# Kernel optimization log

Hardware: AMD Instinct MI355X
Metric: run time of the kernel (lower is better)

## Reference

```python
import jax, jax.numpy as jnp
import numpy as np

B, S, D, U = 4, 2048, 1024, 1024

def setup_inputs() -> dict:
    key = jax.random.key(0)
    k0, k1, k2, k3 = jax.random.split(key, 4)
    scale = 1.0 / np.sqrt(D)  # keep logits sane; Glorot-like magnitude
    return {
        "inputs": jax.random.normal(k0, (B, S, D), dtype=jnp.float32),
        "W_q": jax.random.normal(k1, (D, U), dtype=jnp.float32) * scale,
        "W_k": jax.random.normal(k2, (D, U), dtype=jnp.float32) * scale,
        "W_v": jax.random.normal(k3, (D, U), dtype=jnp.float32) * scale,
    }

def reference(inputs, W_q, W_k, W_v):
    # QKV projections: [B,S,D] @ [D,U] -> [B,S,U]
    q = jnp.einsum("bsd,du->bsu", inputs, W_q)
    k = jnp.einsum("bsd,du->bsu", inputs, W_k)
    v = jnp.einsum("bsd,du->bsu", inputs, W_v)
    # Unscaled attention, as in the source (no 1/sqrt(d) factor)
    scores = jnp.einsum("bqu,bku->bqk", q, k)          # [B,S,S]
    weights = jax.nn.softmax(scores, axis=-1)
    return jnp.einsum("bqk,bku->bqu", weights, v)       # [B,S,U]
```

## Files before the change

kernel.cpp:

```cpp
#include <hip/hip_runtime.h>
#include <cstdint>
#include <cstddef>


typedef unsigned short ushort_t;
typedef _Float16 half_t;
typedef __attribute__((ext_vector_type(8))) short short8;
typedef __attribute__((ext_vector_type(4))) float floatx4;

__device__ inline unsigned short h2u(half_t h) {
  union { half_t h; unsigned short u; } v; v.h = h; return v.u;
}

__device__ __forceinline__ void gload16(const half_t* g, half_t* l) {
  __builtin_amdgcn_global_load_lds(
      (const __attribute__((address_space(1))) unsigned int*)g,
      (__attribute__((address_space(3))) unsigned int*)l, 16, 0, 0);
}

#define BAR() asm volatile("s_barrier" ::: "memory")
#define LGKM0() asm volatile("s_waitcnt lgkmcnt(0)" ::: "memory")
#define VM6() asm volatile("s_waitcnt vmcnt(6)" ::: "memory")
#define VM0() asm volatile("s_waitcnt vmcnt(0)" ::: "memory")

#define MX 8192
#define KCAT 2048

#define XCAT_OFF 0UL
#define WT_OFF   50331648UL
#define S_OFF    0UL
#define QCAT_OFF 69206016UL
#define KCAT_OFF 119537664UL
#define VT_OFF   169869312UL
#define WS_NEED  186646528UL

__global__ __launch_bounds__(256) void k_split_x(const float* __restrict__ X,
                                                 half_t* __restrict__ xcat) {
  long long i = (long long)blockIdx.x * 256 + threadIdx.x;
  float x = X[i];
  half_t h = (half_t)x;
  half_t lo = (half_t)(x - (float)h);
  long long row = i >> 10;
  int col = (int)(i & 1023);
  half_t* r = xcat + row * KCAT;
  r[col] = h;
  r[col + 1024] = lo;
}

__global__ __launch_bounds__(256) void k_split_wt(const float* __restrict__ Wq,
                                                  const float* __restrict__ Wk,
                                                  const float* __restrict__ Wv,
                                                  half_t* __restrict__ wt) {
  __shared__ float tile[64][65];
  const float* W = (blockIdx.z == 0) ? Wq : ((blockIdx.z == 1) ? Wk : Wv);
  half_t* out = wt + (size_t)blockIdx.z * 1024 * KCAT;
  int d0 = blockIdx.y * 64, u0 = blockIdx.x * 64;
  int t = threadIdx.x;
  int tr = t >> 6, tc = t & 63;
  for (int r = 0; r < 64; r += 4)
    tile[r + tr][tc] = W[(size_t)(d0 + r + tr) * 1024 + (u0 + tc)];
  __syncthreads();
  for (int r = 0; r < 64; r += 4) {
    int urow = r + tr, dcol = tc;
    float x = tile[dcol][urow];
    half_t h = (half_t)x;
    half_t* o = out + (size_t)(u0 + urow) * KCAT + d0;
    o[dcol] = h;
    o[dcol + 1024] = h;
  }
}

enum { EP_F32 = 0, EP_QK = 1, EP_VT = 2 };

template <int MODE>
__global__ __launch_bounds__(256, 4) void k_gemm(
    const half_t* __restrict__ A, long long aBatch, int lda,
    const half_t* __restrict__ Bt, long long bBatch, int ldb,
    void* __restrict__ Cout, long long cBatch, int ldc, int K,
    half_t* __restrict__ CoutK) {
  __shared__ __align__(16) half_t As[128 * 64];
  __shared__ __align__(16) half_t Bs[128 * 64];
  const int t = threadIdx.x;
  const int z = blockIdx.z;
  A += (long long)z * aBatch;
  Bt += (long long)z * bBatch;
  const int m0 = blockIdx.y * 128, n0 = blockIdx.x * 128;

  const int w = t >> 6, l = t & 63;
  const int lr = l & 15, quad = l >> 4;
  const int wm = (w >> 1) * 64, wn = (w & 1) * 64;

  const floatx4 fz = {0.f, 0.f, 0.f, 0.f};
  floatx4 acc[4][4];
#pragma unroll
  for (int i = 0; i < 4; i++)
#pragma unroll
    for (int j = 0; j < 4; j++) acc[i][j] = fz;

  const half_t* Ap[4];
  const half_t* Bp[4];
  half_t* ldsA[4];
  half_t* ldsB[4];
#pragma unroll
  for (int s = 0; s < 4; s++) {
    int c = s * 256 + t;
    int row = c >> 3, gq = (c & 7) ^ ((c >> 3) & 7);
    Ap[s] = A + (long long)(m0 + row) * lda + gq * 8;
    Bp[s] = Bt + (long long)(n0 + row) * ldb + gq * 8;
    ldsA[s] = &As[(s * 256 + w * 64) * 8];
    ldsB[s] = &Bs[(s * 256 + w * 64) * 8];
  }

  const int p0 = quad ^ (lr & 7);
  const int p1 = (quad + 4) ^ (lr & 7);
  const int arow = (wm + lr) * 64, brow = (wn + lr) * 64;

  for (int kb = 0; kb < K; kb += 64) {
    __syncthreads();
#pragma unroll
    for (int s = 0; s < 4; s++) {
      gload16(Ap[s] + kb, ldsA[s]);
      gload16(Bp[s] + kb, ldsB[s]);
    }
    __syncthreads();
#pragma unroll
    for (int s = 0; s < 2; s++) {
      const int pp = s ? p1 : p0;
      short8 af[4], bfg[4];
#pragma unroll
      for (int j = 0; j < 4; j++) bfg[j] = *(const short8*)&Bs[brow + j * 1024 + pp * 8];
#pragma unroll
      for (int i = 0; i < 4; i++) af[i] = *(const short8*)&As[arow + i * 1024 + pp * 8];
#pragma unroll
      for (int i = 0; i < 4; i++)
#pragma unroll
        for (int j = 0; j < 4; j++)
          acc[i][j] = __builtin_amdgcn_mfma_f32_16x16x32_f16(af[i], bfg[j], acc[i][j], 0, 0, 0);
    }
  }

#pragma unroll
  for (int i = 0; i < 4; i++) {
#pragma unroll
    for (int j = 0; j < 4; j++) {
#pragma unroll
      for (int r = 0; r < 4; r++) {
        int grow = m0 + wm + i * 16 + quad * 4 + r;
        int gcol = n0 + wn + j * 16 + lr;
        float v = acc[i][j][r];
        if (MODE == EP_F32) {
          float* C = (float*)Cout + (long long)z * cBatch;
          C[(long long)grow * ldc + gcol] = v;
        } else if (MODE == EP_QK) {
          int sel = gcol >> 10;
          int ucol = gcol & 1023;
          half_t h = (half_t)v;
          if (sel == 0) {
            half_t* pq = (half_t*)Cout + (long long)grow * KCAT;
            pq[ucol] = h;
            pq[ucol + 1024] = (half_t)(v - (float)h);
          } else {
            half_t* pk = CoutK + (long long)grow * KCAT;
            pk[ucol] = h;
            pk[ucol + 1024] = h;
          }
        } else {
          half_t* C = (half_t*)Cout;
          int b = grow >> 11, s = grow & 2047;
          C[((long long)b * 1024 + gcol) * 2048 + s] = (half_t)v;
        }
      }
    }
  }
}

template <int MODE>
__global__ __launch_bounds__(512, 2) void k_gemm256(
    const half_t* __restrict__ A, long long aBatch, int lda,
    const half_t* __restrict__ Bt, long long bBatch, int ldb,
    void* __restrict__ Cout, long long cBatch, int ldc, int K,
    half_t* __restrict__ CoutK) {
  __shared__ __align__(16) half_t As[32768];
  __shared__ __align__(16) half_t Bs[32768];
  const int tid = threadIdx.x;
  const int z = blockIdx.z;
  A += (long long)z * aBatch;
  Bt += (long long)z * bBatch;
  const int m0 = blockIdx.y * 256, n0 = blockIdx.x * 256;
  const int w = tid >> 6, l = tid & 63;
  const int lr = l & 15, quad = l >> 4;
  const int wm = w >> 2, wn = w & 3;

  const floatx4 fz = {0.f, 0.f, 0.f, 0.f};
  floatx4 acc[8][4];
#pragma unroll
  for (int i = 0; i < 8; i++)
#pragma unroll
    for (int j = 0; j < 4; j++) acc[i][j] = fz;

  const int r0 = tid >> 2;
  const int gq0 = (tid & 3) ^ ((tid >> 3) & 3);
  const half_t* aS0 = A + (long long)(m0 + r0) * lda + gq0 * 8;
  const half_t* aS1 = aS0 + (long long)128 * lda;
  const half_t* bS0 = Bt + (long long)(n0 + r0) * ldb + gq0 * 8;
  const half_t* bS1 = bS0 + (long long)128 * ldb;
  const int wso = w << 9;

  const int swz = (quad ^ ((lr >> 1) & 3)) << 3;
  const int aBase = wm * 4096 + lr * 32 + swz;
  const int bBase = wn * 2048 + lr * 32 + swz;
  const int NT = K >> 6;

#define SA(BUF, KH, KOFF) do { half_t* d_ = &As[(BUF) * 16384 + (KH) * 8192 + wso]; \
    gload16(aS0 + (KOFF), d_); gload16(aS1 + (KOFF), d_ + 4096); } while (0)
#define SB(BUF, KH, KOFF) do { half_t* d_ = &Bs[(BUF) * 16384 + (KH) * 8192 + wso]; \
    gload16(bS0 + (KOFF), d_); gload16(bS1 + (KOFF), d_ + 4096); } while (0)
#define LDA4(OFF) { const half_t* ap_ = &As[(OFF)]; \
    af0 = *(const short8*)(ap_); af1 = *(const short8*)(ap_ + 512); \
    af2 = *(const short8*)(ap_ + 1024); af3 = *(const short8*)(ap_ + 1536); }
#define LDB4(OFF) { const half_t* bp_ = &Bs[(OFF)]; \
    bf0 = *(const short8*)(bp_); bf1 = *(const short8*)(bp_ + 512); \
    bf2 = *(const short8*)(bp_ + 1024); bf3 = *(const short8*)(bp_ + 1536); }
#define MFMA16(I0) do { \
    acc[(I0) + 0][0] = __builtin_amdgcn_mfma_f32_16x16x32_f16(af0, bf0, acc[(I0) + 0][0], 0, 0, 0); \
    acc[(I0) + 0][1] = __builtin_amdgcn_mfma_f32_16x16x32_f16(af0, bf1, acc[(I0) + 0][1], 0, 0, 0); \
    acc[(I0) + 0][2] = __builtin_amdgcn_mfma_f32_16x16x32_f16(af0, bf2, acc[(I0) + 0][2], 0, 0, 0); \
    acc[(I0) + 0][3] = __builtin_amdgcn_mfma_f32_16x16x32_f16(af0, bf3, acc[(I0) + 0][3], 0, 0, 0); \
    acc[(I0) + 1][0] = __builtin_amdgcn_mfma_f32_16x16x32_f16(af1, bf0, acc[(I0) + 1][0], 0, 0, 0); \
    acc[(I0) + 1][1] = __builtin_amdgcn_mfma_f32_16x16x32_f16(af1, bf1, acc[(I0) + 1][1], 0, 0, 0); \
    acc[(I0) + 1][2] = __builtin_amdgcn_mfma_f32_16x16x32_f16(af1, bf2, acc[(I0) + 1][2], 0, 0, 0); \
    acc[(I0) + 1][3] = __builtin_amdgcn_mfma_f32_16x16x32_f16(af1, bf3, acc[(I0) + 1][3], 0, 0, 0); \
    acc[(I0) + 2][0] = __builtin_amdgcn_mfma_f32_16x16x32_f16(af2, bf0, acc[(I0) + 2][0], 0, 0, 0); \
    acc[(I0) + 2][1] = __builtin_amdgcn_mfma_f32_16x16x32_f16(af2, bf1, acc[(I0) + 2][1], 0, 0, 0); \
    acc[(I0) + 2][2] = __builtin_amdgcn_mfma_f32_16x16x32_f16(af2, bf2, acc[(I0) + 2][2], 0, 0, 0); \
    acc[(I0) + 2][3] = __builtin_amdgcn_mfma_f32_16x16x32_f16(af2, bf3, acc[(I0) + 2][3], 0, 0, 0); \
    acc[(I0) + 3][0] = __builtin_amdgcn_mfma_f32_16x16x32_f16(af3, bf0, acc[(I0) + 3][0], 0, 0, 0); \
    acc[(I0) + 3][1] = __builtin_amdgcn_mfma_f32_16x16x32_f16(af3, bf1, acc[(I0) + 3][1], 0, 0, 0); \
    acc[(I0) + 3][2] = __builtin_amdgcn_mfma_f32_16x16x32_f16(af3, bf2, acc[(I0) + 3][2], 0, 0, 0); \
    acc[(I0) + 3][3] = __builtin_amdgcn_mfma_f32_16x16x32_f16(af3, bf3, acc[(I0) + 3][3], 0, 0, 0); \
  } while (0)

  SB(0, 0, 0); SA(0, 0, 0); SB(0, 1, 32); SA(0, 1, 32);
  SB(1, 0, 64); SA(1, 0, 64); SB(1, 1, 96);
  VM6();
  BAR();

  for (int t = 0; t < NT; ++t) {
    const int buf = t & 1, nbuf = buf ^ 1;
    const int ab = buf * 16384;
    const int kb = t * 64;
    short8 af0, af1, af2, af3, bf0, bf1, bf2, bf3;

    LDA4(ab + aBase);
    LDB4(ab + bBase);
    if (t + 1 < NT) SA(nbuf, 1, kb + 96);
    BAR(); LGKM0();
    __builtin_amdgcn_s_setprio(1); MFMA16(0); __builtin_amdgcn_s_setprio(0);
    BAR();

    LDA4(ab + aBase + 2048);
    if (t + 2 < NT) SB(buf, 0, kb + 128);
    BAR(); LGKM0();
    __builtin_amdgcn_s_setprio(1); MFMA16(4); __builtin_amdgcn_s_setprio(0);
    BAR();

    LDA4(ab + 8192 + aBase);
    LDB4(ab + 8192 + bBase);
    if (t + 2 < NT) SA(buf, 0, kb + 128);
    BAR(); LGKM0();
    __builtin_amdgcn_s_setprio(1); MFMA16(0); __builtin_amdgcn_s_setprio(0);
    BAR();

    LDA4(ab + 8192 + aBase + 2048);
    if (t + 2 < NT) SB(buf, 1, kb + 160);
    if (t < NT - 2) { VM6(); } else if (t == NT - 2) { VM0(); }
    BAR(); LGKM0();
    __builtin_amdgcn_s_setprio(1); MFMA16(4); __builtin_amdgcn_s_setprio(0);
    BAR();
  }

#pragma unroll
  for (int i = 0; i < 8; i++) {
#pragma unroll
    for (int j = 0; j < 4; j++) {
#pragma unroll
      for (int r = 0; r < 4; r++) {
        int grow = m0 + wm * 128 + i * 16 + quad * 4 + r;
        int gcol = n0 + wn * 64 + j * 16 + lr;
        float v = acc[i][j][r];
        if (MODE == EP_F32) {
          float* C = (float*)Cout + (long long)z * cBatch;
          C[(long long)grow * ldc + gcol] = v;
        } else {
          int sel = gcol >> 10;
          int ucol = gcol & 1023;
          half_t h = (half_t)v;
          if (sel == 0) {
            half_t* pq = (half_t*)Cout + (long long)grow * KCAT;
            pq[ucol] = h;
            pq[ucol + 1024] = (half_t)(v - (float)h);
          } else {
            half_t* pk = CoutK + (long long)grow * KCAT;
            pk[ucol] = h;
            pk[ucol + 1024] = h;
          }
        }
      }
    }
  }
#undef SA
#undef SB
#undef LDA4
#undef LDB4
#undef MFMA16
}

__global__ __launch_bounds__(256) void k_softmax(float* __restrict__ Sbuf) {
  long long row = blockIdx.x;
  float* p = Sbuf + row * 2048;
  int t = threadIdx.x;
  float4 v0 = ((const float4*)p)[t];
  float4 v1 = ((const float4*)p)[t + 256];
  float m = fmaxf(fmaxf(fmaxf(v0.x, v0.y), fmaxf(v0.z, v0.w)),
                  fmaxf(fmaxf(v1.x, v1.y), fmaxf(v1.z, v1.w)));
  for (int off = 32; off; off >>= 1) m = fmaxf(m, __shfl_xor(m, off));
  __shared__ float red[8];
  int wv = t >> 6, ln = t & 63;
  if (ln == 0) red[wv] = m;
  __syncthreads();
  m = fmaxf(fmaxf(red[0], red[1]), fmaxf(red[2], red[3]));
  float e0 = __expf(v0.x - m), e1 = __expf(v0.y - m), e2 = __expf(v0.z - m), e3 = __expf(v0.w - m);
  float e4 = __expf(v1.x - m), e5 = __expf(v1.y - m), e6 = __expf(v1.z - m), e7 = __expf(v1.w - m);
  float s = ((e0 + e1) + (e2 + e3)) + ((e4 + e5) + (e6 + e7));
  for (int off = 32; off; off >>= 1) s += __shfl_xor(s, off);
  if (ln == 0) red[4 + wv] = s;
  __syncthreads();
  s = (red[4] + red[5]) + (red[6] + red[7]);
  float inv = 1.0f / s;
  uint2 w0, w1;
  w0.x = (unsigned)h2u((half_t)(e0 * inv)) | ((unsigned)h2u((half_t)(e1 * inv)) << 16);
  w0.y = (unsigned)h2u((half_t)(e2 * inv)) | ((unsigned)h2u((half_t)(e3 * inv)) << 16);
  w1.x = (unsigned)h2u((half_t)(e4 * inv)) | ((unsigned)h2u((half_t)(e5 * inv)) << 16);
  w1.y = (unsigned)h2u((half_t)(e6 * inv)) | ((unsigned)h2u((half_t)(e7 * inv)) << 16);
  ((uint2*)p)[t] = w0;
  ((uint2*)p)[t + 256] = w1;
}

extern "C" void kernel_launch(void* const* d_in, const int* in_sizes, int n_in,
                              void* d_out, int out_size, void* d_ws, size_t ws_size,
                              hipStream_t stream) {
  (void)in_sizes; (void)n_in; (void)out_size;
  if (ws_size < WS_NEED) return;

  const float* X = (const float*)d_in[0];
  const float* Wq = (const float*)d_in[1];
  const float* Wk = (const float*)d_in[2];
  const float* Wv = (const float*)d_in[3];
  char* ws = (char*)d_ws;
  half_t* xcat = (half_t*)(ws + XCAT_OFF);
  half_t* wt = (half_t*)(ws + WT_OFF);
  float* Sbuf = (float*)(ws + S_OFF);
  half_t* qcat = (half_t*)(ws + QCAT_OFF);
  half_t* kcat = (half_t*)(ws + KCAT_OFF);
  half_t* vt = (half_t*)(ws + VT_OFF);
  float* out = (float*)d_out;

  k_split_x<<<dim3(MX * 1024 / 256), dim3(256), 0, stream>>>(X, xcat);
  k_split_wt<<<dim3(16, 16, 3), dim3(256), 0, stream>>>(Wq, Wk, Wv, wt);

  k_gemm256<EP_QK><<<dim3(8, 32, 1), dim3(512), 0, stream>>>(
      xcat, 0LL, KCAT, wt, 0LL, KCAT, qcat, 0LL, 0, KCAT, kcat);

  k_gemm<EP_VT><<<dim3(8, 64, 1), dim3(256), 0, stream>>>(
      xcat, 0LL, KCAT, wt + 2 * 1024 * KCAT, 0LL, KCAT, vt, 0LL, 0, 1024, nullptr);

  k_gemm256<EP_F32><<<dim3(8, 8, 4), dim3(512), 0, stream>>>(
      qcat, (long long)2048 * KCAT, KCAT, kcat, (long long)2048 * KCAT, KCAT,
      Sbuf, (long long)2048 * 2048, 2048, KCAT, nullptr);

  k_softmax<<<dim3(8192), dim3(256), 0, stream>>>(Sbuf);

  k_gemm<EP_F32><<<dim3(8, 16, 4), dim3(256), 0, stream>>>(
      (const half_t*)Sbuf, (long long)2048 * 4096, 4096,
      vt, (long long)1024 * 2048, 2048,
      out, (long long)2048 * 1024, 1024, 2048, nullptr);
}
```

Measured before the change: 336.7 us.

## Stage GEMM epilogues through LDS and split-K the PV GEMM with atomics

The 256x256 GEMM epilogue now stages accumulators through swizzled LDS so the Q/K and fp32 score outputs are written with wide vectorized stores instead of scattered scalar stores. The final weights-times-V GEMM moves from the 128-tile kernel to the 256-tile kernel, with K split in two across blockIdx.z and partial sums combined into a pre-zeroed output via atomicAdd. This targets poor store coalescing and low tile reuse in the final GEMM. The cost is an extra zeroing pass, atomic traffic on the output, and an accumulation order that is no longer deterministic.

```diff
diff --git a/kernel.cpp b/kernel.cpp
--- a/kernel.cpp
+++ b/kernel.cpp
@@ -33,6 +33,13 @@
 #define KCAT_OFF 119537664UL
 #define VT_OFF   169869312UL
 #define WS_NEED  186646528UL
+
+__global__ __launch_bounds__(256) void k_zero(float* __restrict__ p, long long n4) {
+  long long i = (long long)blockIdx.x * 256 + threadIdx.x;
+  const floatx4 z = {0.f, 0.f, 0.f, 0.f};
+  long long stride = (long long)gridDim.x * 256;
+  for (; i < n4; i += stride) ((floatx4*)p)[i] = z;
+}
 
 __global__ __launch_bounds__(256) void k_split_x(const float* __restrict__ X,
                                                  half_t* __restrict__ xcat) {
@@ -70,7 +77,7 @@
   }
 }
 
-enum { EP_F32 = 0, EP_QK = 1, EP_VT = 2 };
+enum { EP_F32 = 0, EP_QK = 1, EP_VT = 2, EP_ATOMIC = 3 };
 
 template <int MODE>
 __global__ __launch_bounds__(256, 4) void k_gemm(
@@ -180,12 +187,15 @@
     const half_t* __restrict__ Bt, long long bBatch, int ldb,
     void* __restrict__ Cout, long long cBatch, int ldc, int K,
     half_t* __restrict__ CoutK) {
-  __shared__ __align__(16) half_t As[32768];
-  __shared__ __align__(16) half_t Bs[32768];
+  __shared__ __align__(16) half_t LDS[65536];
+  half_t* As = LDS;
+  half_t* Bs = LDS + 32768;
   const int tid = threadIdx.x;
   const int z = blockIdx.z;
-  A += (long long)z * aBatch;
-  Bt += (long long)z * bBatch;
+  int zb = z, kOff = 0;
+  if (MODE == EP_ATOMIC) { zb = z >> 1; kOff = (z & 1) * 1024; }
+  A += (long long)zb * aBatch + kOff;
+  Bt += (long long)zb * bBatch + kOff;
   const int m0 = blockIdx.y * 256, n0 = blockIdx.x * 256;
   const int w = tid >> 6, l = tid & 63;
   const int lr = l & 15, quad = l >> 4;
@@ -279,34 +289,79 @@
     BAR();
   }
 
-#pragma unroll
-  for (int i = 0; i < 8; i++) {
-#pragma unroll
-    for (int j = 0; j < 4; j++) {
-#pragma unroll
-      for (int r = 0; r < 4; r++) {
-        int grow = m0 + wm * 128 + i * 16 + quad * 4 + r;
-        int gcol = n0 + wn * 64 + j * 16 + lr;
-        float v = acc[i][j][r];
-        if (MODE == EP_F32) {
-          float* C = (float*)Cout + (long long)z * cBatch;
-          C[(long long)grow * ldc + gcol] = v;
-        } else {
-          int sel = gcol >> 10;
-          int ucol = gcol & 1023;
-          half_t h = (half_t)v;
-          if (sel == 0) {
-            half_t* pq = (half_t*)Cout + (long long)grow * KCAT;
-            pq[ucol] = h;
-            pq[ucol + 1024] = (half_t)(v - (float)h);
-          } else {
-            half_t* pk = CoutK + (long long)grow * KCAT;
-            pk[ucol] = h;
-            pk[ucol + 1024] = h;
+  BAR();
+  half_t* wreg = &LDS[w * 8192];
+
+  if (MODE == EP_QK) {
+    const int sel = n0 >> 10;
+    const int ncol0 = (n0 & 1023) + wn * 64;
+    half_t* dbase = (sel == 0) ? (half_t*)Cout : CoutK;
+    const long long rb = (long long)(m0 + wm * 128);
+#pragma unroll
+    for (int round = 0; round < 2; ++round) {
+#pragma unroll
+      for (int i = 0; i < 8; i++)
+#pragma unroll
+        for (int j = 0; j < 4; j++)
+#pragma unroll
+          for (int r = 0; r < 4; r++) {
+            int row = i * 16 + quad * 4 + r;
+            int col = j * 16 + lr;
+            float v = acc[i][j][r];
+            half_t hv = (half_t)v;
+            half_t val = (round == 0) ? hv
+                         : (sel == 0 ? (half_t)(v - (float)hv) : hv);
+            wreg[row * 64 + (((col >> 3) ^ (row & 7)) << 3) + (col & 7)] = val;
           }
-        }
+#pragma unroll
+      for (int k2 = 0; k2 < 16; ++k2) {
+        int cid = l + 64 * k2;
+        int row = cid >> 3, q = cid & 7;
+        short8 vv = *(const short8*)&wreg[row * 64 + ((q ^ (row & 7)) << 3)];
+        half_t* dst = dbase + (rb + row) * KCAT + ncol0 + q * 8 + round * 1024;
+        *(short8*)dst = vv;
       }
     }
+  } else if (MODE == EP_F32) {
+    float* wreg32 = (float*)wreg;
+    float* C = (float*)Cout + (long long)zb * cBatch;
+#pragma unroll
+    for (int hh = 0; hh < 2; ++hh) {
+#pragma unroll
+      for (int i2 = 0; i2 < 4; i2++)
+#pragma unroll
+        for (int j = 0; j < 4; j++)
+#pragma unroll
+          for (int r = 0; r < 4; r++) {
+            int i = hh * 4 + i2;
+            int row64 = i2 * 16 + quad * 4 + r;
+            int col = j * 16 + lr;
+            int c4 = col >> 2;
+            wreg32[row64 * 64 + ((c4 ^ (row64 & 7)) << 2) + (col & 3)] =
+                acc[i][j][r];
+          }
+      long long rbase = (long long)(m0 + wm * 128 + hh * 64);
+#pragma unroll
+      for (int k2 = 0; k2 < 16; ++k2) {
+        int cid = l + 64 * k2;
+        int row64 = cid >> 4, q = cid & 15;
+        floatx4 vv = *(const floatx4*)&wreg32[row64 * 64 + ((q ^ (row64 & 7)) << 2)];
+        float* dst = C + (rbase + row64) * ldc + n0 + wn * 64 + q * 4;
+        *(floatx4*)dst = vv;
+      }
+    }
+  } else {
+    float* C = (float*)Cout + (long long)zb * cBatch;
+#pragma unroll
+    for (int i = 0; i < 8; i++)
+#pragma unroll
+      for (int j = 0; j < 4; j++)
+#pragma unroll
+        for (int r = 0; r < 4; r++) {
+          int grow = m0 + wm * 128 + i * 16 + quad * 4 + r;
+          int gcol = n0 + wn * 64 + j * 16 + lr;
+          atomicAdd(&C[(long long)grow * ldc + gcol], acc[i][j][r]);
+        }
   }
 #undef SA
 #undef SB
@@ -365,6 +420,8 @@
   half_t* vt = (half_t*)(ws + VT_OFF);
   float* out = (float*)d_out;
 
+  k_zero<<<dim3(1024), dim3(256), 0, stream>>>(out, (long long)MX * 1024 / 4);
+
   k_split_x<<<dim3(MX * 1024 / 256), dim3(256), 0, stream>>>(X, xcat);
   k_split_wt<<<dim3(16, 16, 3), dim3(256), 0, stream>>>(Wq, Wk, Wv, wt);
 
@@ -380,8 +437,8 @@
 
   k_softmax<<<dim3(8192), dim3(256), 0, stream>>>(Sbuf);
 
-  k_gemm<EP_F32><<<dim3(8, 16, 4), dim3(256), 0, stream>>>(
+  k_gemm256<EP_ATOMIC><<<dim3(4, 8, 8), dim3(512), 0, stream>>>(
       (const half_t*)Sbuf, (long long)2048 * 4096, 4096,
       vt, (long long)1024 * 2048, 2048,
-      out, (long long)2048 * 1024, 1024, 2048, nullptr);
-}
+      out, (long long)2048 * 1024, 1024, 1024, nullptr);
+}
```

After: 431.2 us. 28.1% more time.

## Split-K the PV GEMM into two partials and pack Q/K hi-lo stores

Applied to the files above, without the earlier changes.

The final weights·V GEMM is split along K into two halves, doubling the grid from 512 to 1024 blocks so more CUs have work. Each half writes an fp32 partial into reused workspace, and a new elementwise kernel sums the two partials into the output. This trades better occupancy for an extra kernel launch and extra write and read traffic on the partial buffers. Separately, the QK projection epilogue now interleaves the hi/lo (or hi/hi) half pairs and writes each pair as one 32-bit store instead of two scattered 16-bit stores; the pairing stays consistent for the QK^T contraction.

```diff
diff --git a/kernel.cpp b/kernel.cpp
--- a/kernel.cpp
+++ b/kernel.cpp
@@ -31,6 +31,7 @@
 #define S_OFF    0UL
 #define QCAT_OFF 69206016UL
 #define KCAT_OFF 119537664UL
+#define PART_OFF QCAT_OFF
 #define VT_OFF   169869312UL
 #define WS_NEED  186646528UL
 
@@ -70,7 +71,22 @@
   }
 }
 
-enum { EP_F32 = 0, EP_QK = 1, EP_VT = 2 };
+__global__ __launch_bounds__(256) void k_addout(const float* __restrict__ part,
+                                                float* __restrict__ out,
+                                                long long n4) {
+  long long i = (long long)blockIdx.x * 256 + threadIdx.x;
+  long long stride = (long long)gridDim.x * 256;
+  const floatx4* p0 = (const floatx4*)part;
+  const floatx4* p1 = (const floatx4*)(part + (long long)MX * 1024);
+  floatx4* o4 = (floatx4*)out;
+  for (; i < n4; i += stride) {
+    floatx4 a = p0[i];
+    floatx4 b = p1[i];
+    o4[i] = a + b;
+  }
+}
+
+enum { EP_F32 = 0, EP_QK = 1, EP_VT = 2, EP_PART = 3 };
 
 template <int MODE>
 __global__ __launch_bounds__(256, 4) void k_gemm(
@@ -82,8 +98,10 @@
   __shared__ __align__(16) half_t Bs[128 * 64];
   const int t = threadIdx.x;
   const int z = blockIdx.z;
-  A += (long long)z * aBatch;
-  Bt += (long long)z * bBatch;
+  int zb = z, kOff = 0;
+  if (MODE == EP_PART) { zb = z >> 1; kOff = (z & 1) << 10; }
+  A += (long long)zb * aBatch + kOff;
+  Bt += (long long)zb * bBatch + kOff;
   const int m0 = blockIdx.y * 128, n0 = blockIdx.x * 128;
 
   const int w = t >> 6, l = t & 63;
@@ -149,21 +167,12 @@
         int gcol = n0 + wn + j * 16 + lr;
         float v = acc[i][j][r];
         if (MODE == EP_F32) {
-          float* C = (float*)Cout + (long long)z * cBatch;
+          float* C = (float*)Cout + (long long)zb * cBatch;
           C[(long long)grow * ldc + gcol] = v;
-        } else if (MODE == EP_QK) {
-          int sel = gcol >> 10;
-          int ucol = gcol & 1023;
-          half_t h = (half_t)v;
-          if (sel == 0) {
-            half_t* pq = (half_t*)Cout + (long long)grow * KCAT;
-            pq[ucol] = h;
-            pq[ucol + 1024] = (half_t)(v - (float)h);
-          } else {
-            half_t* pk = CoutK + (long long)grow * KCAT;
-            pk[ucol] = h;
-            pk[ucol + 1024] = h;
-          }
+        } else if (MODE == EP_PART) {
+          float* C = (float*)Cout + (long long)(z & 1) * ((long long)MX * 1024) +
+                     (long long)zb * cBatch;
+          C[(long long)grow * ldc + gcol] = v;
         } else {
           half_t* C = (half_t*)Cout;
           int b = grow >> 11, s = grow & 2047;
@@ -295,15 +304,17 @@
           int sel = gcol >> 10;
           int ucol = gcol & 1023;
           half_t h = (half_t)v;
+          unsigned hu = h2u(h);
+          unsigned val;
+          half_t* base;
           if (sel == 0) {
-            half_t* pq = (half_t*)Cout + (long long)grow * KCAT;
-            pq[ucol] = h;
-            pq[ucol + 1024] = (half_t)(v - (float)h);
+            val = hu | ((unsigned)h2u((half_t)(v - (float)h)) << 16);
+            base = (half_t*)Cout;
           } else {
-            half_t* pk = CoutK + (long long)grow * KCAT;
-            pk[ucol] = h;
-            pk[ucol + 1024] = h;
+            val = hu | (hu << 16);
+            base = CoutK;
           }
+          *(unsigned*)(base + (long long)grow * KCAT + 2 * ucol) = val;
         }
       }
     }
@@ -362,6 +373,7 @@
   float* Sbuf = (float*)(ws + S_OFF);
   half_t* qcat = (half_t*)(ws + QCAT_OFF);
   half_t* kcat = (half_t*)(ws + KCAT_OFF);
+  float* part = (float*)(ws + PART_OFF);
   half_t* vt = (half_t*)(ws + VT_OFF);
   float* out = (float*)d_out;
 
@@ -380,8 +392,11 @@
 
   k_softmax<<<dim3(8192), dim3(256), 0, stream>>>(Sbuf);
 
-  k_gemm<EP_F32><<<dim3(8, 16, 4), dim3(256), 0, stream>>>(
+  k_gemm<EP_PART><<<dim3(8, 16, 8), dim3(256), 0, stream>>>(
       (const half_t*)Sbuf, (long long)2048 * 4096, 4096,
       vt, (long long)1024 * 2048, 2048,
-      out, (long long)2048 * 1024, 1024, 2048, nullptr);
-}
+      part, (long long)2048 * 1024, 1024, 1024, nullptr);
+
+  k_addout<<<dim3(2048), dim3(256), 0, stream>>>(part, out,
+                                                 (long long)MX * 1024 / 4);
+}
```

Result: slower. 359.6 us (+6.8%).

## Remap GEMM block indices per XCD and pack hi/lo half stores

Applied to the files above, without the earlier changes.

Adds an XCD-aware block index remapping to both GEMM kernels. Blocks dispatched round-robin across chiplets then work on neighbouring output tiles, so A/B tiles are more likely to be reused from each chiplet's L2. The QK epilogue of the 256 kernel now interleaves the hi/lo (or duplicated) halves and writes them as one 32-bit store, replacing two scattered 16-bit stores. The unused EP_QK path is dropped from the 128 kernel. The remap hardcodes a grid x-dimension of 8 and divisibility assumptions, and the interleaved layout relies on producer and consumer agreeing on the new order.

```diff
diff --git a/kernel.cpp b/kernel.cpp
--- a/kernel.cpp
+++ b/kernel.cpp
@@ -33,6 +33,14 @@
 #define KCAT_OFF 119537664UL
 #define VT_OFF   169869312UL
 #define WS_NEED  186646528UL
+
+#define XCD_REMAP(BX, BY, BZ)                                              \
+  const int fbid_ = blockIdx.x + 8 * (blockIdx.y + gridDim.y * blockIdx.z); \
+  const int xj_ = fbid_ & 7, xi_ = fbid_ >> 3;                              \
+  const int BX = ((xj_ & 1) << 2) | (xi_ & 3);                              \
+  const int nrow_ = (xj_ >> 1) * ((gridDim.y * gridDim.z) >> 2) + (xi_ >> 2);\
+  const int BY = nrow_ % gridDim.y;                                         \
+  const int BZ = nrow_ / gridDim.y;
 
 __global__ __launch_bounds__(256) void k_split_x(const float* __restrict__ X,
                                                  half_t* __restrict__ xcat) {
@@ -81,10 +89,10 @@
   __shared__ __align__(16) half_t As[128 * 64];
   __shared__ __align__(16) half_t Bs[128 * 64];
   const int t = threadIdx.x;
-  const int z = blockIdx.z;
+  XCD_REMAP(bx, by, z);
   A += (long long)z * aBatch;
   Bt += (long long)z * bBatch;
-  const int m0 = blockIdx.y * 128, n0 = blockIdx.x * 128;
+  const int m0 = by * 128, n0 = bx * 128;
 
   const int w = t >> 6, l = t & 63;
   const int lr = l & 15, quad = l >> 4;
@@ -151,19 +159,6 @@
         if (MODE == EP_F32) {
           float* C = (float*)Cout + (long long)z * cBatch;
           C[(long long)grow * ldc + gcol] = v;
-        } else if (MODE == EP_QK) {
-          int sel = gcol >> 10;
-          int ucol = gcol & 1023;
-          half_t h = (half_t)v;
-          if (sel == 0) {
-            half_t* pq = (half_t*)Cout + (long long)grow * KCAT;
-            pq[ucol] = h;
-            pq[ucol + 1024] = (half_t)(v - (float)h);
-          } else {
-            half_t* pk = CoutK + (long long)grow * KCAT;
-            pk[ucol] = h;
-            pk[ucol + 1024] = h;
-          }
         } else {
           half_t* C = (half_t*)Cout;
           int b = grow >> 11, s = grow & 2047;
@@ -183,10 +178,10 @@
   __shared__ __align__(16) half_t As[32768];
   __shared__ __align__(16) half_t Bs[32768];
   const int tid = threadIdx.x;
-  const int z = blockIdx.z;
+  XCD_REMAP(bx, by, z);
   A += (long long)z * aBatch;
   Bt += (long long)z * bBatch;
-  const int m0 = blockIdx.y * 256, n0 = blockIdx.x * 256;
+  const int m0 = by * 256, n0 = bx * 256;
   const int w = tid >> 6, l = tid & 63;
   const int lr = l & 15, quad = l >> 4;
   const int wm = w >> 2, wn = w & 3;
@@ -295,15 +290,17 @@
           int sel = gcol >> 10;
           int ucol = gcol & 1023;
           half_t h = (half_t)v;
+          unsigned hu = h2u(h);
+          unsigned val;
+          half_t* base;
           if (sel == 0) {
-            half_t* pq = (half_t*)Cout + (long long)grow * KCAT;
-            pq[ucol] = h;
-            pq[ucol + 1024] = (half_t)(v - (float)h);
+            val = hu | ((unsigned)h2u((half_t)(v - (float)h)) << 16);
+            base = (half_t*)Cout;
           } else {
-            half_t* pk = CoutK + (long long)grow * KCAT;
-            pk[ucol] = h;
-            pk[ucol + 1024] = h;
+            val = hu | (hu << 16);
+            base = CoutK;
           }
+          *(unsigned*)(base + (long long)grow * KCAT + 2 * ucol) = val;
         }
       }
     }
```

Result: faster. 318.3 us (-5.5%).
